# Performance work log

Hardware: AMD Instinct MI355X
Metric: run time of the kernel (lower is better)

Reference implementation:

```python
import jax, jax.numpy as jnp
import numpy as np

B, N, E = 2, 2048, 1024   # batch, seq_len, embed_dim (= hidden_dim)
H, HD = 16, 64            # num_heads, head_dim


def setup_inputs() -> dict:
    key = jax.random.key(0)
    ks = jax.random.split(key, 6)
    w = lambda k: jax.random.normal(k, (E, E), jnp.float32) * 0.02
    return {
        "x": jax.random.normal(ks[0], (B, N, E), jnp.float32),
        "Wq": w(ks[1]), "bq": jnp.zeros((E,), jnp.float32),
        "Wk": w(ks[2]), "bk": jnp.zeros((E,), jnp.float32),
        "Wv": w(ks[3]), "bv": jnp.zeros((E,), jnp.float32),
        "Wu": w(ks[4]), "bu": jnp.zeros((E,), jnp.float32),
        "Wo": w(ks[5]), "bo": jnp.zeros((E,), jnp.float32),
        "ln_g": jnp.ones((E,), jnp.float32),
        "ln_b": jnp.zeros((E,), jnp.float32),
    }


def reference(x, Wq, bq, Wk, bk, Wv, bv, Wu, bu, Wo, bo, ln_g, ln_b):
    # projections (torch Linear: x @ W.T + b)
    q = x @ Wq.T + bq
    k = x @ Wk.T + bk
    v = jax.nn.silu(x @ Wv.T + bv)   # uv_act = swish
    u = jax.nn.silu(x @ Wu.T + bu)
    # split heads: [B, N, H*HD] -> [B, H, N, HD]
    split = lambda t: t.reshape(B, N, H, HD).transpose(0, 2, 1, 3)
    q, k, v = split(q), split(k), split(v)
    # non-softmax attention: ReLU on scaled energy (no causal mask)
    energy = jnp.einsum("bhnd,bhmd->bhnm", q, k) / jnp.float32(np.sqrt(HD))
    energy = jax.nn.relu(energy)
    out = jnp.einsum("bhnm,bhmd->bhnd", energy, v)
    # merge heads: [B, H, N, HD] -> [B, N, H*HD]
    out = out.transpose(0, 2, 1, 3).reshape(B, N, H * HD)
    # layernorm over hidden_dim
    mu = out.mean(-1, keepdims=True)
    var = out.var(-1, keepdims=True)
    out = (out - mu) * jax.lax.rsqrt(var + 1e-5) * ln_g + ln_b
    # gate and output projection
    out = u * out
    return out @ Wo.T + bo
```

## Files before the change

### kernel.cpp

```cpp
#include <hip/hip_runtime.h>
#include <stdint.h>

typedef unsigned short u16;
typedef __attribute__((ext_vector_type(8))) short short8;
typedef __attribute__((ext_vector_type(4))) short short4v;
typedef __attribute__((ext_vector_type(4))) float floatx4;
typedef __attribute__((ext_vector_type(4))) int intx4;

#define B_ 2
#define N_ 2048
#define E_ 1024
#define H_ 16
#define HD_ 64
#define M_TOT (B_ * N_)

__device__ __forceinline__ float bf2f(u16 h) {
    union { unsigned u; float f; } c; c.u = ((unsigned)h) << 16; return c.f;
}
__device__ __forceinline__ u16 f2bf(float f) {
    union { float f; unsigned u; } c; c.f = f;
    unsigned r = c.u + 0x7FFFu + ((c.u >> 16) & 1u);
    return (u16)(r >> 16);
}
__device__ __forceinline__ float silu_f(float x) { return x / (1.f + __expf(-x)); }

__device__ __forceinline__ void gll16(const void* g, void* l) {
    __builtin_amdgcn_global_load_lds(
        (const __attribute__((address_space(1))) void*)g,
        (__attribute__((address_space(3))) void*)l,
        16, 0, 0);
}

__device__ __forceinline__ short4v relu_pack(floatx4 s) {
    union { float f; unsigned u; } c0, c1, c2, c3;
    c0.f = fmaxf(s[0], 0.f); c1.f = fmaxf(s[1], 0.f);
    c2.f = fmaxf(s[2], 0.f); c3.f = fmaxf(s[3], 0.f);
    unsigned lo = __builtin_amdgcn_perm(c1.u + 0x8000u, c0.u + 0x8000u, 0x07060302);
    unsigned hi = __builtin_amdgcn_perm(c3.u + 0x8000u, c2.u + 0x8000u, 0x07060302);
    union { unsigned v[2]; short4v s4; } r; r.v[0] = lo; r.v[1] = hi;
    return r.s4;
}

__launch_bounds__(256, 4)
__global__ void cvt6(const float* __restrict__ s0, const float* __restrict__ s1,
                     const float* __restrict__ s2, const float* __restrict__ s3,
                     const float* __restrict__ s4, const float* __restrict__ s5,
                     u16* __restrict__ d0, u16* __restrict__ d1,
                     u16* __restrict__ d2, u16* __restrict__ d3,
                     u16* __restrict__ d4, u16* __restrict__ d5)
{
    const int z = blockIdx.z;
    if (z > 0 && blockIdx.x >= E_ * E_ / 2048) return;
    const float* src = (z == 0) ? s0 : (z == 1) ? s1 : (z == 2) ? s2
                     : (z == 3) ? s3 : (z == 4) ? s4 : s5;
    u16* dst         = (z == 0) ? d0 : (z == 1) ? d1 : (z == 2) ? d2
                     : (z == 3) ? d3 : (z == 4) ? d4 : d5;
    const int i = (blockIdx.x * 256 + threadIdx.x) * 8;
    floatx4 a = *(const floatx4*)(src + i);
    floatx4 b = *(const floatx4*)(src + i + 4);
    union { u16 h[8]; intx4 v; } o;
    o.h[0] = f2bf(a[0]); o.h[1] = f2bf(a[1]); o.h[2] = f2bf(a[2]); o.h[3] = f2bf(a[3]);
    o.h[4] = f2bf(b[0]); o.h[5] = f2bf(b[1]); o.h[6] = f2bf(b[2]); o.h[7] = f2bf(b[3]);
    *(intx4*)(dst + i) = o.v;
}

#define NTILES (E_ / 64)

#define LDA_FRAGS(mlo, BUF)                                                        \
    _Pragma("unroll")                                                              \
    for (int mi = 0; mi < 4; mi++) {                                               \
        af[(mlo) + mi][0] = *(const short8*)&lds[(BUF)*16384 + raA + ((mlo)+mi)*512];        \
        af[(mlo) + mi][1] = *(const short8*)&lds[(BUF)*16384 + raA + 4096 + ((mlo)+mi)*512]; \
    }

#define LDB_FRAGS(blo, BUF)                                                        \
    _Pragma("unroll")                                                              \
    for (int bn = 0; bn < 2; bn++) {                                               \
        bfr[bn][0] = *(const short8*)&lds[32768 + (BUF)*16384 + raB + ((blo)+bn)*512];        \
        bfr[bn][1] = *(const short8*)&lds[32768 + (BUF)*16384 + raB + 4096 + ((blo)+bn)*512]; \
    }

#define MFMAQ(mlo, blo)                                                            \
    _Pragma("unroll")                                                              \
    for (int mi = 0; mi < 4; mi++)                                                 \
        _Pragma("unroll")                                                          \
        for (int bn = 0; bn < 2; bn++) {                                           \
            acc[(mlo)+mi][(blo)+bn] = __builtin_amdgcn_mfma_f32_16x16x32_bf16(     \
                af[(mlo)+mi][0], bfr[bn][0], acc[(mlo)+mi][(blo)+bn], 0, 0, 0);    \
            acc[(mlo)+mi][(blo)+bn] = __builtin_amdgcn_mfma_f32_16x16x32_bf16(     \
                af[(mlo)+mi][1], bfr[bn][1], acc[(mlo)+mi][(blo)+bn], 0, 0, 0);    \
        }

#define STAGE_AH(t2, h, BUFX)                                                      \
    if ((t2) < NTILES) {                                                           \
        gll16(As + (size_t)(h)*128*E_ + (t2)*64,      &lds[(BUFX)*16384 + (h)*8192 + wid*512]);        \
        gll16(As + (size_t)(h)*128*E_ + (t2)*64 + 32, &lds[(BUFX)*16384 + (h)*8192 + 4096 + wid*512]); \
    }

#define STAGE_BH(t1, h, BUFX)                                                      \
    if ((t1) < NTILES) {                                                           \
        gll16(Bs + (size_t)(h)*128*E_ + (t1)*64,      &lds[32768 + (BUFX)*16384 + (h)*8192 + wid*512]);        \
        gll16(Bs + (size_t)(h)*128*E_ + (t1)*64 + 32, &lds[32768 + (BUFX)*16384 + (h)*8192 + 4096 + wid*512]); \
    }

#define TILE(t, BUF) {                                                             \
    LDA_FRAGS(0, BUF); LDB_FRAGS(0, BUF);                                          \
    STAGE_BH((t)+1, 0, (BUF)^1);                                                   \
    __builtin_amdgcn_s_barrier();                                                  \
    __builtin_amdgcn_s_setprio(1); MFMAQ(0, 0); __builtin_amdgcn_s_setprio(0);     \
    __builtin_amdgcn_s_barrier();                                                  \
    LDA_FRAGS(4, BUF);                                                             \
    STAGE_BH((t)+1, 1, (BUF)^1);                                                   \
    __builtin_amdgcn_s_barrier();                                                  \
    __builtin_amdgcn_s_setprio(1); MFMAQ(4, 0); __builtin_amdgcn_s_setprio(0);     \
    __builtin_amdgcn_s_barrier();                                                  \
    LDB_FRAGS(2, BUF);                                                             \
    STAGE_AH((t)+2, 0, BUF);                                                       \
    __builtin_amdgcn_s_barrier();                                                  \
    __builtin_amdgcn_s_setprio(1); MFMAQ(4, 2); __builtin_amdgcn_s_setprio(0);     \
    __builtin_amdgcn_s_barrier();                                                  \
    STAGE_AH((t)+2, 1, BUF);                                                       \
    __builtin_amdgcn_s_barrier();                                                  \
    __builtin_amdgcn_s_setprio(1); MFMAQ(0, 2); __builtin_amdgcn_s_setprio(0);     \
    asm volatile("s_waitcnt vmcnt(4)" ::: "memory");                               \
    __builtin_amdgcn_s_barrier();                                                  \
}

__launch_bounds__(512, 2)
__global__ void gemm8p(const u16* __restrict__ A,
                       const u16* __restrict__ W0, const u16* __restrict__ W1,
                       const u16* __restrict__ W2, const u16* __restrict__ W3,
                       const float* __restrict__ bi0, const float* __restrict__ bi1,
                       const float* __restrict__ bi2, const float* __restrict__ bi3,
                       u16* __restrict__ O0, u16* __restrict__ O1,
                       u16* __restrict__ O2, u16* __restrict__ O3,
                       int actmask, int scalemask)
{
    __shared__ u16 lds[65536];

    const int z = blockIdx.z;
    const u16* Wp   = (z == 0) ? W0 : (z == 1) ? W1 : (z == 2) ? W2 : W3;
    const float* Bi = (z == 0) ? bi0 : (z == 1) ? bi1 : (z == 2) ? bi2 : bi3;
    u16* Out        = (z == 0) ? O0 : (z == 1) ? O1 : (z == 2) ? O2 : O3;
    const bool act = (actmask >> z) & 1;
    const float osc = ((scalemask >> z) & 1) ? 0.125f : 1.0f;

    const int tid = threadIdx.x;
    const int wid = tid >> 6, lane = tid & 63, quad = lane >> 4, l16 = lane & 15;
    const int wm = wid >> 2, wn = wid & 3;
    const int m0 = blockIdx.y * 256;
    const int n0 = blockIdx.x * 256;

    const int swz = ((l16 >> 3) & 1) * 16;
    const int raA = wm * 8192 + l16 * 32 + ((quad * 8) ^ swz);
    const int raB = (wn >> 1) * 8192 + ((wn & 1) * 64 + l16) * 32 + ((quad * 8) ^ swz);

    const int srow_s = tid >> 2;
    const int sce = ((tid & 3) * 8) ^ (((tid >> 5) & 1) * 16);
    const u16* As = A  + (size_t)(m0 + srow_s) * E_ + sce;
    const u16* Bs = Wp + (size_t)(n0 + srow_s) * E_ + sce;

    floatx4 acc[8][4];
    const floatx4 fz = {0.f, 0.f, 0.f, 0.f};
#pragma unroll
    for (int mi = 0; mi < 8; mi++)
#pragma unroll
        for (int bn = 0; bn < 4; bn++) acc[mi][bn] = fz;

    short8 af[8][2], bfr[2][2];

    gll16(As,                  &lds[0     + wid*512]);
    gll16(As + 32,             &lds[4096  + wid*512]);
    gll16(As + 128*E_,         &lds[8192  + wid*512]);
    gll16(As + 128*E_ + 32,    &lds[12288 + wid*512]);
    gll16(Bs,                  &lds[32768 +  0    + wid*512]);
    gll16(Bs + 32,             &lds[32768 + 4096  + wid*512]);
    gll16(Bs + 128*E_,         &lds[32768 + 8192  + wid*512]);
    gll16(Bs + 128*E_ + 32,    &lds[32768 + 12288 + wid*512]);
    gll16(As + 64,             &lds[16384 +  0    + wid*512]);
    gll16(As + 96,             &lds[16384 + 4096  + wid*512]);
    gll16(As + 128*E_ + 64,    &lds[16384 + 8192  + wid*512]);
    gll16(As + 128*E_ + 96,    &lds[16384 + 12288 + wid*512]);
    asm volatile("s_waitcnt vmcnt(4)" ::: "memory");
    __builtin_amdgcn_s_barrier();

    for (int tt = 0; tt < NTILES; tt += 2) {
        TILE(tt, 0);
        TILE(tt + 1, 1);
    }

    float bias_v[4];
#pragma unroll
    for (int bn = 0; bn < 4; bn++) bias_v[bn] = Bi[n0 + wn * 64 + bn * 16 + l16];

#pragma unroll
    for (int mi = 0; mi < 8; mi++) {
        const int row = m0 + wm * 128 + mi * 16 + quad * 4;
#pragma unroll
        for (int bn = 0; bn < 4; bn++) {
            const int col = n0 + wn * 64 + bn * 16 + l16;
#pragma unroll
            for (int r = 0; r < 4; r++) {
                float v = acc[mi][bn][r] + bias_v[bn];
                if (act) v = silu_f(v);
                v *= osc;
                Out[(size_t)(row + r) * E_ + col] = f2bf(v);
            }
        }
    }
}

__launch_bounds__(256, 2)
__global__ void gemm_out(const u16* __restrict__ A, const u16* __restrict__ W,
                         const float* __restrict__ Bi, float* __restrict__ Out,
                         int K)
{
    __shared__ u16 a_lds[64 * 32];
    __shared__ u16 b_lds[128 * 32];

    const int t    = threadIdx.x;
    const int wave = t >> 6, lane = t & 63, quad = lane >> 4, l16 = lane & 15;
    const int m0 = blockIdx.y * 64;
    const int n0 = blockIdx.x * 128;

    floatx4 acc[4][2];
    const floatx4 fz = {0.f, 0.f, 0.f, 0.f};
    for (int i = 0; i < 4; i++)
        for (int j = 0; j < 2; j++) acc[i][j] = fz;

    const int ar = t >> 2;
    const int ac = (t & 3) * 8;
    const u16* Ag0 = A + (size_t)(m0 + ar) * K + ac;
    const u16* Bg0 = W + (size_t)(n0 + ar) * K + ac;
    const u16* Bg1 = W + (size_t)(n0 + 64 + ar) * K + ac;
    u16* al0 = a_lds + wave * 512;
    u16* bl0 = b_lds + wave * 512;
    u16* bl1 = b_lds + 2048 + wave * 512;

    for (int k0 = 0; k0 < K; k0 += 32) {
        __syncthreads();
        gll16(Ag0 + k0, al0);
        gll16(Bg0 + k0, bl0);
        gll16(Bg1 + k0, bl1);
        __syncthreads();

        short8 af[4], bfr[2];
        for (int i = 0; i < 4; i++)
            af[i]  = *(const short8*)&a_lds[(i * 16 + l16) * 32 + quad * 8];
        for (int j = 0; j < 2; j++)
            bfr[j] = *(const short8*)&b_lds[(wave * 32 + j * 16 + l16) * 32 + quad * 8];
        for (int i = 0; i < 4; i++)
            for (int j = 0; j < 2; j++)
                acc[i][j] = __builtin_amdgcn_mfma_f32_16x16x32_bf16(af[i], bfr[j], acc[i][j], 0, 0, 0);
    }

    float bias_v[2];
    for (int j = 0; j < 2; j++) bias_v[j] = Bi[n0 + wave * 32 + j * 16 + l16];

    for (int i = 0; i < 4; i++) {
        const int row = m0 + i * 16 + quad * 4;
        for (int j = 0; j < 2; j++) {
            const int col = n0 + wave * 32 + j * 16 + l16;
            for (int r = 0; r < 4; r++)
                Out[(size_t)(row + r) * E_ + col] = acc[i][j][r] + bias_v[j];
        }
    }
}

#define LK 72
#define LV 72
#define KSPLIT 2
#define KCHUNK (N_ / KSPLIT)

__launch_bounds__(256, 2)
__global__ void attn(const u16* __restrict__ Q, const u16* __restrict__ Kk,
                     const u16* __restrict__ V,
                     u16* __restrict__ P0, u16* __restrict__ P1)
{
    __shared__ u16 k_lds[64 * LK];
    __shared__ u16 v_lds[64 * LV];

    const int bh = blockIdx.y;
    const int b = bh >> 4, h = bh & 15;
    const int z = blockIdx.z;
    u16* __restrict__ Oa = (z == 0) ? P0 : P1;
    const int key_base = z * KCHUNK;

    const int t = threadIdx.x;
    const int wave = t >> 6, lane = t & 63, quad = lane >> 4, l16 = lane & 15;
    const int q0 = blockIdx.x * 256 + wave * 64;
    const size_t base = (size_t)b * N_ * E_ + h * HD_;

    short8 aq[4][2];
    for (int mi = 0; mi < 4; mi++)
        for (int ks = 0; ks < 2; ks++)
            aq[mi][ks] = *(const short8*)(Q + base + (size_t)(q0 + mi * 16 + l16) * E_ + ks * 32 + quad * 8);

    floatx4 o[4][4];
    const floatx4 fz = {0.f, 0.f, 0.f, 0.f};
    for (int mi = 0; mi < 4; mi++)
        for (int nd = 0; nd < 4; nd++) o[mi][nd] = fz;

    const int srow = t >> 2, sseg = (t & 3) * 16;
    const int prow = (srow & 32) + (((srow >> 2) & 1) << 4)
                   + (((srow >> 3) & 3) << 2) + (srow & 3);
    const u16* Ksrc = Kk + base + (size_t)(key_base + srow) * E_ + sseg;
    u16* kdst = &k_lds[prow * LK + sseg];
    const u16* Vsrc = V + base + (size_t)(key_base + srow) * E_ + sseg;

    for (int kt = 0; kt < KCHUNK / 64; kt++) {
        __syncthreads();
        const u16* kg = Ksrc + (size_t)(kt * 64) * E_;
        const u16* vg = Vsrc + (size_t)(kt * 64) * E_;
        intx4 kv0 = *(const intx4*)(kg);
        intx4 kv1 = *(const intx4*)(kg + 8);
        intx4 vv0 = *(const intx4*)(vg);
        intx4 vv1 = *(const intx4*)(vg + 8);
        *(intx4*)(kdst)     = kv0;
        *(intx4*)(kdst + 8) = kv1;
        const u16* v0p = (const u16*)&vv0;
        const u16* v1p = (const u16*)&vv1;
        for (int i = 0; i < 8; i++) {
            v_lds[(sseg + i) * LV + srow]     = v0p[i];
            v_lds[(sseg + 8 + i) * LV + srow] = v1p[i];
        }
        __syncthreads();

        for (int g = 0; g < 2; g++) {
            short8 ka[2][2];
            for (int tp = 0; tp < 2; tp++)
                for (int ks = 0; ks < 2; ks++)
                    ka[tp][ks] = *(const short8*)&k_lds[(g * 32 + tp * 16 + l16) * LK + ks * 32 + quad * 8];
            short8 bv[4];
            for (int nd = 0; nd < 4; nd++)
                bv[nd] = *(const short8*)&v_lds[(nd * 16 + l16) * LV + g * 32 + quad * 8];

            for (int mi = 0; mi < 4; mi++) {
                floatx4 c0 = __builtin_amdgcn_mfma_f32_16x16x32_bf16(ka[0][0], aq[mi][0], fz, 0, 0, 0);
                c0 = __builtin_amdgcn_mfma_f32_16x16x32_bf16(ka[0][1], aq[mi][1], c0, 0, 0, 0);
                floatx4 c1 = __builtin_amdgcn_mfma_f32_16x16x32_bf16(ka[1][0], aq[mi][0], fz, 0, 0, 0);
                c1 = __builtin_amdgcn_mfma_f32_16x16x32_bf16(ka[1][1], aq[mi][1], c1, 0, 0, 0);
                union { short4v h[2]; short8 s8; } sf;
                sf.h[0] = relu_pack(c0);
                sf.h[1] = relu_pack(c1);
                for (int nd = 0; nd < 4; nd++)
                    o[mi][nd] = __builtin_amdgcn_mfma_f32_16x16x32_bf16(sf.s8, bv[nd], o[mi][nd], 0, 0, 0);
            }
        }
    }

    for (int mi = 0; mi < 4; mi++)
        for (int nd = 0; nd < 4; nd++)
            for (int r = 0; r < 4; r++)
                Oa[(size_t)(b * N_ + q0 + mi * 16 + quad * 4 + r) * E_ + h * HD_ + nd * 16 + l16] =
                    f2bf(o[mi][nd][r]);
}

__launch_bounds__(256, 4)
__global__ void ln_gate(const u16* __restrict__ P0, const u16* __restrict__ P1,
                        const u16* __restrict__ U,
                        const float* __restrict__ G, const float* __restrict__ Bb,
                        u16* __restrict__ Out)
{
    const int row = blockIdx.x;
    const int t = threadIdx.x;
    const size_t idx = (size_t)row * E_ + t * 4;
    const short4v a0 = *(const short4v*)(P0 + idx);
    const short4v a1 = *(const short4v*)(P1 + idx);
    floatx4 v;
    for (int i = 0; i < 4; i++)
        v[i] = bf2f((u16)a0[i]) + bf2f((u16)a1[i]);
    float s  = v[0] + v[1] + v[2] + v[3];
    float ss = v[0] * v[0] + v[1] * v[1] + v[2] * v[2] + v[3] * v[3];
    for (int off = 32; off; off >>= 1) {
        s  += __shfl_down(s, off, 64);
        ss += __shfl_down(ss, off, 64);
    }
    __shared__ float red[8];
    const int wave = t >> 6, lane = t & 63;
    if (lane == 0) { red[wave] = s; red[4 + wave] = ss; }
    __syncthreads();
    const float S  = red[0] + red[1] + red[2] + red[3];
    const float SS = red[4] + red[5] + red[6] + red[7];
    const float mu  = S * (1.f / E_);
    const float var = SS * (1.f / E_) - mu * mu;
    const float rstd = rsqrtf(var + 1e-5f);

    short4v outv;
    for (int i = 0; i < 4; i++) {
        const int e = t * 4 + i;
        float y = (v[i] - mu) * rstd * G[e] + Bb[e];
        y *= bf2f(U[idx + i]);
        outv[i] = (short)f2bf(y);
    }
    *(short4v*)(Out + idx) = outv;
}

extern "C" void kernel_launch(void* const* d_in, const int* in_sizes, int n_in,
                              void* d_out, int out_size, void* d_ws, size_t ws_size,
                              hipStream_t stream)
{
    const float* x   = (const float*)d_in[0];
    const float* Wq  = (const float*)d_in[1];
    const float* bq  = (const float*)d_in[2];
    const float* Wk  = (const float*)d_in[3];
    const float* bk  = (const float*)d_in[4];
    const float* Wv  = (const float*)d_in[5];
    const float* bv  = (const float*)d_in[6];
    const float* Wu  = (const float*)d_in[7];
    const float* bu  = (const float*)d_in[8];
    const float* Wo  = (const float*)d_in[9];
    const float* bo  = (const float*)d_in[10];
    const float* lng = (const float*)d_in[11];
    const float* lnb = (const float*)d_in[12];

    char* ws = (char*)d_ws;
    u16*  qw  = (u16*)(ws);
    u16*  kw  = (u16*)(ws + 8388608);
    u16*  vw  = (u16*)(ws + 16777216);
    u16*  uw  = (u16*)(ws + 25165824);
    u16*  p0  = (u16*)(ws + 33554432);
    u16*  p1  = (u16*)(ws + 41943040);
    u16*  xb  = (u16*)(ws + 50331648);
    u16*  wbq = (u16*)(ws + 58720256);
    u16*  wbk = (u16*)(ws + 60817408);
    u16*  wbv = (u16*)(ws + 62914560);
    u16*  wbu = (u16*)(ws + 65011712);
    u16*  wbo = (u16*)(ws + 67108864);
    u16*  gw  = (u16*)(ws);

    float* out = (float*)d_out;

    cvt6<<<dim3(M_TOT * E_ / 2048, 1, 6), dim3(256, 1, 1), 0, stream>>>(
        x, Wq, Wk, Wv, Wu, Wo, xb, wbq, wbk, wbv, wbu, wbo);
    gemm8p<<<dim3(E_ / 256, M_TOT / 256, 4), dim3(512, 1, 1), 0, stream>>>(
        xb, wbq, wbk, wbv, wbu, bq, bk, bv, bu, qw, kw, vw, uw, 0xC, 0x1);
    attn<<<dim3(N_ / 256, B_ * H_, KSPLIT), dim3(256, 1, 1), 0, stream>>>(qw, kw, vw, p0, p1);
    ln_gate<<<dim3(M_TOT, 1, 1), dim3(256, 1, 1), 0, stream>>>(p0, p1, uw, lng, lnb, gw);
    gemm_out<<<dim3(E_ / 128, M_TOT / 64, 1), dim3(256, 1, 1), 0, stream>>>(gw, wbo, bo, out, E_);
}
```

Before: 210.1 us.

## Multi-buffer LDS tiles in output GEMM and attention to overlap loads

The output-projection GEMM now uses a three-stage LDS ring, issuing async global-to-LDS loads two tiles ahead and waiting on vmcnt instead of double __syncthreads. The attention kernel double-buffers its K/V LDS tiles, holding the next tile's loads in registers during the MFMA work and writing them to the alternate buffer afterwards. Both changes aim to hide global memory latency behind matrix math. In exchange they use more LDS and registers, which may reduce occupancy, and the hand-written vmcnt accounting must stay correct.

```diff
diff --git a/kernel.cpp b/kernel.cpp
--- a/kernel.cpp
+++ b/kernel.cpp
@@ -215,8 +215,8 @@
                          const float* __restrict__ Bi, float* __restrict__ Out,
                          int K)
 {
-    __shared__ u16 a_lds[64 * 32];
-    __shared__ u16 b_lds[128 * 32];
+    __shared__ u16 a_lds[3][64 * 32];
+    __shared__ u16 b_lds[3][128 * 32];
 
     const int t    = threadIdx.x;
     const int wave = t >> 6, lane = t & 63, quad = lane >> 4, l16 = lane & 15;
@@ -233,26 +233,45 @@
     const u16* Ag0 = A + (size_t)(m0 + ar) * K + ac;
     const u16* Bg0 = W + (size_t)(n0 + ar) * K + ac;
     const u16* Bg1 = W + (size_t)(n0 + 64 + ar) * K + ac;
-    u16* al0 = a_lds + wave * 512;
-    u16* bl0 = b_lds + wave * 512;
-    u16* bl1 = b_lds + 2048 + wave * 512;
-
-    for (int k0 = 0; k0 < K; k0 += 32) {
-        __syncthreads();
-        gll16(Ag0 + k0, al0);
-        gll16(Bg0 + k0, bl0);
-        gll16(Bg1 + k0, bl1);
-        __syncthreads();
-
+
+    const int nt = K / 32;
+
+#define GO_STAGE(tt, bi) {                                      \
+        gll16(Ag0 + (tt) * 32, &a_lds[bi][wave * 512]);         \
+        gll16(Bg0 + (tt) * 32, &b_lds[bi][wave * 512]);         \
+        gll16(Bg1 + (tt) * 32, &b_lds[bi][2048 + wave * 512]); }
+
+    GO_STAGE(0, 0);
+    GO_STAGE(1, 1);
+    asm volatile("s_waitcnt vmcnt(3)" ::: "memory");
+    __builtin_amdgcn_s_barrier();
+
+    for (int tt = 0; tt < nt; tt++) {
+        const int bi = tt % 3;
+        if (tt + 2 < nt) {
+            const int b2 = (tt + 2) % 3;
+            GO_STAGE(tt + 2, b2);
+        }
         short8 af[4], bfr[2];
+#pragma unroll
         for (int i = 0; i < 4; i++)
-            af[i]  = *(const short8*)&a_lds[(i * 16 + l16) * 32 + quad * 8];
+            af[i]  = *(const short8*)&a_lds[bi][(i * 16 + l16) * 32 + quad * 8];
+#pragma unroll
         for (int j = 0; j < 2; j++)
-            bfr[j] = *(const short8*)&b_lds[(wave * 32 + j * 16 + l16) * 32 + quad * 8];
+            bfr[j] = *(const short8*)&b_lds[bi][(wave * 32 + j * 16 + l16) * 32 + quad * 8];
+#pragma unroll
         for (int i = 0; i < 4; i++)
+#pragma unroll
             for (int j = 0; j < 2; j++)
                 acc[i][j] = __builtin_amdgcn_mfma_f32_16x16x32_bf16(af[i], bfr[j], acc[i][j], 0, 0, 0);
-    }
+        if (tt + 2 < nt) {
+            asm volatile("s_waitcnt vmcnt(3)" ::: "memory");
+        } else {
+            asm volatile("s_waitcnt vmcnt(0)" ::: "memory");
+        }
+        __builtin_amdgcn_s_barrier();
+    }
+#undef GO_STAGE
 
     float bias_v[2];
     for (int j = 0; j < 2; j++) bias_v[j] = Bi[n0 + wave * 32 + j * 16 + l16];
@@ -271,14 +290,15 @@
 #define LV 72
 #define KSPLIT 2
 #define KCHUNK (N_ / KSPLIT)
+#define NKT (KCHUNK / 64)
 
 __launch_bounds__(256, 2)
 __global__ void attn(const u16* __restrict__ Q, const u16* __restrict__ Kk,
                      const u16* __restrict__ V,
                      u16* __restrict__ P0, u16* __restrict__ P1)
 {
-    __shared__ u16 k_lds[64 * LK];
-    __shared__ u16 v_lds[64 * LV];
+    __shared__ u16 k_lds[2][64 * LK];
+    __shared__ u16 v_lds[2][64 * LV];
 
     const int bh = blockIdx.y;
     const int b = bh >> 4, h = bh & 15;
@@ -305,35 +325,45 @@
     const int prow = (srow & 32) + (((srow >> 2) & 1) << 4)
                    + (((srow >> 3) & 3) << 2) + (srow & 3);
     const u16* Ksrc = Kk + base + (size_t)(key_base + srow) * E_ + sseg;
-    u16* kdst = &k_lds[prow * LK + sseg];
     const u16* Vsrc = V + base + (size_t)(key_base + srow) * E_ + sseg;
-
-    for (int kt = 0; kt < KCHUNK / 64; kt++) {
-        __syncthreads();
-        const u16* kg = Ksrc + (size_t)(kt * 64) * E_;
-        const u16* vg = Vsrc + (size_t)(kt * 64) * E_;
-        intx4 kv0 = *(const intx4*)(kg);
-        intx4 kv1 = *(const intx4*)(kg + 8);
-        intx4 vv0 = *(const intx4*)(vg);
-        intx4 vv1 = *(const intx4*)(vg + 8);
-        *(intx4*)(kdst)     = kv0;
-        *(intx4*)(kdst + 8) = kv1;
+    const int kofs = prow * LK + sseg;
+
+    intx4 kv0 = *(const intx4*)(Ksrc);
+    intx4 kv1 = *(const intx4*)(Ksrc + 8);
+    intx4 vv0 = *(const intx4*)(Vsrc);
+    intx4 vv1 = *(const intx4*)(Vsrc + 8);
+    {
+        *(intx4*)(&k_lds[0][kofs])     = kv0;
+        *(intx4*)(&k_lds[0][kofs + 8]) = kv1;
         const u16* v0p = (const u16*)&vv0;
         const u16* v1p = (const u16*)&vv1;
         for (int i = 0; i < 8; i++) {
-            v_lds[(sseg + i) * LV + srow]     = v0p[i];
-            v_lds[(sseg + 8 + i) * LV + srow] = v1p[i];
-        }
+            v_lds[0][(sseg + i) * LV + srow]     = v0p[i];
+            v_lds[0][(sseg + 8 + i) * LV + srow] = v1p[i];
+        }
+    }
+
+    for (int kt = 0; kt < NKT; kt++) {
         __syncthreads();
+        const int cur = kt & 1;
+
+        if (kt + 1 < NKT) {
+            const u16* kg = Ksrc + (size_t)((kt + 1) * 64) * E_;
+            const u16* vg = Vsrc + (size_t)((kt + 1) * 64) * E_;
+            kv0 = *(const intx4*)(kg);
+            kv1 = *(const intx4*)(kg + 8);
+            vv0 = *(const intx4*)(vg);
+            vv1 = *(const intx4*)(vg + 8);
+        }
 
         for (int g = 0; g < 2; g++) {
             short8 ka[2][2];
             for (int tp = 0; tp < 2; tp++)
                 for (int ks = 0; ks < 2; ks++)
-                    ka[tp][ks] = *(const short8*)&k_lds[(g * 32 + tp * 16 + l16) * LK + ks * 32 + quad * 8];
+                    ka[tp][ks] = *(const short8*)&k_lds[cur][(g * 32 + tp * 16 + l16) * LK + ks * 32 + quad * 8];
             short8 bv[4];
             for (int nd = 0; nd < 4; nd++)
-                bv[nd] = *(const short8*)&v_lds[(nd * 16 + l16) * LV + g * 32 + quad * 8];
+                bv[nd] = *(const short8*)&v_lds[cur][(nd * 16 + l16) * LV + g * 32 + quad * 8];
 
             for (int mi = 0; mi < 4; mi++) {
                 floatx4 c0 = __builtin_amdgcn_mfma_f32_16x16x32_bf16(ka[0][0], aq[mi][0], fz, 0, 0, 0);
@@ -345,6 +375,18 @@
                 sf.h[1] = relu_pack(c1);
                 for (int nd = 0; nd < 4; nd++)
                     o[mi][nd] = __builtin_amdgcn_mfma_f32_16x16x32_bf16(sf.s8, bv[nd], o[mi][nd], 0, 0, 0);
+            }
+        }
+
+        if (kt + 1 < NKT) {
+            const int nxt = cur ^ 1;
+            *(intx4*)(&k_lds[nxt][kofs])     = kv0;
+            *(intx4*)(&k_lds[nxt][kofs + 8]) = kv1;
+            const u16* v0p = (const u16*)&vv0;
+            const u16* v1p = (const u16*)&vv1;
+            for (int i = 0; i < 8; i++) {
+                v_lds[nxt][(sseg + i) * LV + srow]     = v0p[i];
+                v_lds[nxt][(sseg + 8 + i) * LV + srow] = v1p[i];
             }
         }
     }
```

New measurement: 207.6 us. About the same (-1.2%).
